# Optimization experiments

Hardware: AMD Instinct MI355X
Metric: run time of the kernel (lower is better)

## Reference

```python
import jax, jax.numpy as jnp
import numpy as np

N, E, B = 150000, 600000, 1024
F_IN, F_HID = 78, 312          # 78 * 2**output_dim_power_0(=2)
OUT_DIM = 128
L, VOCAB, EMB = 1000, 26, 128  # num_features_xt+1 = 26 embedding rows
NF, KS = 8, 8                  # 2**n_filters_power, 2**kernel_size_power
CONV_FLAT = NF * (EMB - KS + 1)  # 8*121 = 968
K_HOPS = 2
SLOPE = 0.01                   # torch leaky_relu default

def _lin(k, i, o):
    s = 1.0 / np.sqrt(i)
    kw, kb = jax.random.split(k)
    return (jax.random.uniform(kw, (i, o), jnp.float32, -s, s),
            jax.random.uniform(kb, (o,), jnp.float32, -s, s))

def setup_inputs() -> dict:
    key = jax.random.key(0)
    ks = jax.random.split(key, 12)
    x = jax.random.normal(ks[0], (N, F_IN), jnp.float32)
    edge_index = jax.random.randint(ks[1], (2, E), 0, N)
    batch = (jnp.arange(N) * B) // N            # sorted graph ids, all B graphs nonempty
    target = jax.random.randint(ks[2], (B, L), 0, VOCAB)
    sgc_w, sgc_b = _lin(ks[3], F_IN, F_HID)
    fcg1_w, fcg1_b = _lin(ks[4], F_HID, OUT_DIM)
    emb_table = jax.random.normal(ks[5], (VOCAB, EMB), jnp.float32)
    sc = 1.0 / np.sqrt(L * KS)
    conv_w = jax.random.uniform(ks[6], (NF, L, KS), jnp.float32, -sc, sc)  # OIW
    conv_b = jax.random.uniform(ks[7], (NF,), jnp.float32, -sc, sc)
    fcxt_w, fcxt_b = _lin(ks[8], CONV_FLAT, OUT_DIM)
    fc1_w, fc1_b = _lin(ks[9], 2 * OUT_DIM, 1024)
    fc2_w, fc2_b = _lin(ks[10], 1024, 512)
    out_w, out_b = _lin(ks[11], 512, 1)
    return dict(x=x, sgc_w=sgc_w, sgc_b=sgc_b, fcg1_w=fcg1_w, fcg1_b=fcg1_b,
                emb_table=emb_table, conv_w=conv_w, conv_b=conv_b,
                fcxt_w=fcxt_w, fcxt_b=fcxt_b, fc1_w=fc1_w, fc1_b=fc1_b,
                fc2_w=fc2_w, fc2_b=fc2_b, out_w=out_w, out_b=out_b,
                edge_index=edge_index, batch=batch, target=target)

def reference(x, sgc_w, sgc_b, fcg1_w, fcg1_b, emb_table, conv_w, conv_b,
              fcxt_w, fcxt_b, fc1_w, fc1_b, fc2_w, fc2_b, out_w, out_b,
              edge_index, batch, target):
    # --- SGConv: K-hop symmetric-normalized propagation with self-loops, then linear ---
    loop = jnp.arange(N)
    src = jnp.concatenate([edge_index[0], loop])
    dst = jnp.concatenate([edge_index[1], loop])
    deg = jax.ops.segment_sum(jnp.ones_like(src, jnp.float32), dst, num_segments=N)
    dinv = jnp.where(deg > 0, jax.lax.rsqrt(deg), 0.0)
    norm = (dinv[src] * dinv[dst])[:, None]
    h = x
    for _ in range(K_HOPS):
        h = jax.ops.segment_sum(h[src] * norm, dst, num_segments=N)  # [N, F]
    h = jax.nn.leaky_relu(h @ sgc_w + sgc_b, SLOPE)                  # [N, 312]
    # --- global max pool per graph + fc_g1 ---
    g = jax.ops.segment_max(h, batch, num_segments=B)                # [B, 312]
    g = jax.nn.leaky_relu(g @ fcg1_w + fcg1_b, SLOPE)                # [B, 128]
    # --- protein branch: embed -> Conv1d(in=1000) over embed axis -> flatten -> fc ---
    emb = emb_table[target]                                          # [B, 1000, 128]
    conv = jax.lax.conv_general_dilated(emb, conv_w, (1,), 'VALID',
                                        dimension_numbers=('NCW', 'OIW', 'NCW'))
    conv = conv + conv_b[None, :, None]                              # [B, 8, 121]
    xt = conv.reshape(B, CONV_FLAT) @ fcxt_w + fcxt_b                # [B, 128]
    # --- head ---
    xc = jnp.concatenate([g, xt], axis=1)                            # [B, 256]
    xc = jax.nn.relu(xc @ fc1_w + fc1_b)
    xc = jax.nn.relu(xc @ fc2_w + fc2_b)
    return xc @ out_w + out_b                                        # [B, 1]
```

## Files before the change

### kernel.cpp

```cpp
#include <hip/hip_runtime.h>

#define N_NODES 150000
#define N_EDGES 600000
#define BATCH   1024
#define F_IN    78
#define F_HID   312
#define OUT_DIMW 128
#define SEQ_L   1000
#define VOCAB   26
#define EMB     128
#define NF      8
#define KS      8
#define CONV_WO 121
#define CONV_FLAT 968
#define SK      208
#define SLOPE   0.01f
#define KEY_NEGMAX ((int)0x80800000)
#define SCAN_NBLK ((N_NODES + 255) / 256)

#define KPU  96
#define NT   20
#define BSW_HALF (3 * NT * 64 * 8)
#define M_PAD 150016

typedef __attribute__((ext_vector_type(8))) short bf8;
typedef __attribute__((ext_vector_type(4))) float f4;

__device__ __forceinline__ short f2bf(float f) {
  unsigned u = __float_as_uint(f);
  return (short)((u + 0x7fffu + ((u >> 16) & 1u)) >> 16);
}
__device__ __forceinline__ float bf2f(short h) {
  return __uint_as_float(((unsigned)(unsigned short)h) << 16);
}
__device__ __forceinline__ unsigned packsplit(float v) {
  short h = f2bf(v);
  short l = f2bf(v - bf2f(h));
  return ((unsigned)(unsigned short)h << 16) | (unsigned)(unsigned short)l;
}

__device__ __forceinline__ int fkey(float v) {
  int i = __float_as_int(v);
  return i >= 0 ? i : (i ^ 0x7fffffff);
}
__device__ __forceinline__ float fdec(int k) {
  return __int_as_float(k >= 0 ? k : (k ^ 0x7fffffff));
}

__global__ void k_zero_i(int* __restrict__ p, int n) {
  int i = blockIdx.x * blockDim.x + threadIdx.x;
  if (i < n) p[i] = 0;
}

__global__ void k_deg(const int* __restrict__ dst, int* __restrict__ deg) {
  int e = blockIdx.x * blockDim.x + threadIdx.x;
  if (e < N_EDGES) atomicAdd(&deg[dst[e]], 1);
}

__global__ void k_dinv(const int* __restrict__ deg, float* __restrict__ dinv) {
  int i = blockIdx.x * blockDim.x + threadIdx.x;
  if (i < N_NODES) dinv[i] = rsqrtf((float)(deg[i] + 1));
}

__global__ __launch_bounds__(256) void k_scan1(const int* __restrict__ deg, int* __restrict__ rowptr,
                                               int* __restrict__ bsum) {
  __shared__ int s[256];
  int tid = threadIdx.x;
  int i = blockIdx.x * 256 + tid;
  int v = (i < N_NODES) ? deg[i] : 0;
  s[tid] = v;
  __syncthreads();
  int x = v;
  for (int o = 1; o < 256; o <<= 1) {
    int t = (tid >= o) ? s[tid - o] : 0;
    __syncthreads();
    x += t; s[tid] = x;
    __syncthreads();
  }
  if (i < N_NODES) rowptr[i] = x - v;
  if (tid == 255) bsum[blockIdx.x] = x;
}

__global__ __launch_bounds__(1024) void k_scan2(int* __restrict__ bsum) {
  __shared__ int s[1024];
  int tid = threadIdx.x;
  int v = (tid < SCAN_NBLK) ? bsum[tid] : 0;
  s[tid] = v;
  __syncthreads();
  int x = v;
  for (int o = 1; o < 1024; o <<= 1) {
    int t = (tid >= o) ? s[tid - o] : 0;
    __syncthreads();
    x += t; s[tid] = x;
    __syncthreads();
  }
  if (tid < SCAN_NBLK) bsum[tid] = x - v;
}

__global__ __launch_bounds__(256) void k_scan3(int* __restrict__ rowptr, const int* __restrict__ bsum,
                                               int* __restrict__ cnt) {
  int i = blockIdx.x * 256 + threadIdx.x;
  if (i < N_NODES) { rowptr[i] += bsum[blockIdx.x]; cnt[i] = 0; }
  if (i == 0) rowptr[N_NODES] = N_EDGES;
}

__global__ void k_fillcsr(const int* __restrict__ src, const int* __restrict__ dst,
                          const int* __restrict__ rowptr, int* __restrict__ cnt,
                          int* __restrict__ csr) {
  int e = blockIdx.x * blockDim.x + threadIdx.x;
  if (e < N_EDGES) {
    int d = dst[e];
    int pos = rowptr[d] + atomicAdd(&cnt[d], 1);
    csr[pos] = src[e];
  }
}

template<int HOP1>
__global__ __launch_bounds__(256) void k_pull(const int* __restrict__ rowptr,
                        const int* __restrict__ csr, const float* __restrict__ dinv,
                        const float* __restrict__ p, void* __restrict__ outv) {
  int dv = (int)((blockIdx.x * 256 + threadIdx.x) >> 6);
  if (dv >= N_NODES) return;
  int d = __builtin_amdgcn_readfirstlane(dv);
  int lane = threadIdx.x & 63;
  int j0 = rowptr[d], j1 = rowptr[d + 1];
  bool act = lane < 39;
  float dd = dinv[d];
  float2 aA = make_float2(0.f, 0.f), aB = aA, aC = aA, aD = aA;
  if (act) {
    float2 v = ((const float2*)(p + (size_t)d * F_IN))[lane];
    float c0 = HOP1 ? dd : 1.f;
    aA.x = c0 * v.x; aA.y = c0 * v.y;
  }
  int j = j0;
  for (; j + 3 < j1; j += 4) {
    int s0 = csr[j], s1 = csr[j + 1], s2 = csr[j + 2], s3 = csr[j + 3];
    float c0 = HOP1 ? dinv[s0] : 1.f, c1 = HOP1 ? dinv[s1] : 1.f;
    float c2 = HOP1 ? dinv[s2] : 1.f, c3 = HOP1 ? dinv[s3] : 1.f;
    if (act) {
      float2 u0 = ((const float2*)(p + (size_t)s0 * F_IN))[lane];
      float2 u1 = ((const float2*)(p + (size_t)s1 * F_IN))[lane];
      float2 u2 = ((const float2*)(p + (size_t)s2 * F_IN))[lane];
      float2 u3 = ((const float2*)(p + (size_t)s3 * F_IN))[lane];
      aA.x += c0 * u0.x; aA.y += c0 * u0.y;
      aB.x += c1 * u1.x; aB.y += c1 * u1.y;
      aC.x += c2 * u2.x; aC.y += c2 * u2.y;
      aD.x += c3 * u3.x; aD.y += c3 * u3.y;
    }
  }
  if (j + 1 < j1) {
    int s0 = csr[j], s1 = csr[j + 1];
    float c0 = HOP1 ? dinv[s0] : 1.f, c1 = HOP1 ? dinv[s1] : 1.f;
    if (act) {
      float2 u0 = ((const float2*)(p + (size_t)s0 * F_IN))[lane];
      float2 u1 = ((const float2*)(p + (size_t)s1 * F_IN))[lane];
      aA.x += c0 * u0.x; aA.y += c0 * u0.y;
      aB.x += c1 * u1.x; aB.y += c1 * u1.y;
    }
    j += 2;
  }
  if (j < j1) {
    int s0 = csr[j];
    float c0 = HOP1 ? dinv[s0] : 1.f;
    if (act) {
      float2 u0 = ((const float2*)(p + (size_t)s0 * F_IN))[lane];
      aC.x += c0 * u0.x; aC.y += c0 * u0.y;
    }
  }
  if (HOP1) {
    if (act) {
      float cs = dd * dd;
      ((float2*)((float*)outv + (size_t)d * F_IN))[lane] =
          make_float2(cs * (aA.x + aB.x + aC.x + aD.x), cs * (aA.y + aB.y + aC.y + aD.y));
    }
  } else {
    if (lane < 48) {
      float vx = dd * (aA.x + aB.x + aC.x + aD.x);
      float vy = dd * (aA.y + aB.y + aC.y + aD.y);
      uint2 pk = make_uint2(packsplit(vx), packsplit(vy));
      ((uint2*)((unsigned*)outv + (size_t)d * KPU))[lane] = pk;
    }
  }
}

__global__ __launch_bounds__(256) void k_gemm_sk(const float* __restrict__ A, const float* __restrict__ B,
                        float* __restrict__ Cp, int M, int N, int K, int kc) {
  __shared__ float As[16][33];
  __shared__ float Bs[16][68];
  int bm = blockIdx.x * 32, bn = blockIdx.y * 64;
  int k0s = blockIdx.z * kc;
  int k1s = min(K, k0s + kc);
  int tid = threadIdx.x;
  int tx = tid & 15, ty = tid >> 4;
  float acc[2][4] = {};
  for (int k0 = k0s; k0 < k1s; k0 += 16) {
    {
      int i2 = tid * 2;
      int m = i2 >> 4, k = i2 & 15;
      float2 av = make_float2(0.f, 0.f);
      const float* Ap = A + (size_t)(bm + m) * K + k0 + k;
      if (k0 + k + 1 < k1s)      av = *(const float2*)Ap;
      else if (k0 + k < k1s)     av.x = Ap[0];
      As[k][m] = av.x; As[k + 1][m] = av.y;
    }
    {
      int i4 = tid * 4;
      int kr = i4 >> 6, n = i4 & 63;
      float4 bv = make_float4(0.f, 0.f, 0.f, 0.f);
      if (k0 + kr < k1s) bv = *(const float4*)(B + (size_t)(k0 + kr) * N + bn + n);
      *(float4*)&Bs[kr][n] = bv;
    }
    __syncthreads();
#pragma unroll
    for (int kk = 0; kk < 16; kk++) {
      float a0 = As[kk][ty * 2], a1 = As[kk][ty * 2 + 1];
      float4 b = *(const float4*)&Bs[kk][tx * 4];
      acc[0][0] += a0 * b.x; acc[0][1] += a0 * b.y; acc[0][2] += a0 * b.z; acc[0][3] += a0 * b.w;
      acc[1][0] += a1 * b.x; acc[1][1] += a1 * b.y; acc[1][2] += a1 * b.z; acc[1][3] += a1 * b.w;
    }
    __syncthreads();
  }
#pragma unroll
  for (int im = 0; im < 2; im++) {
    int m = bm + ty * 2 + im;
    float4 v = make_float4(acc[im][0], acc[im][1], acc[im][2], acc[im][3]);
    *(float4*)(Cp + ((size_t)blockIdx.z * M + m) * N + bn + tx * 4) = v;
  }
}

template<int ACT>
__global__ void k_sumact(const float* __restrict__ Cp, int S, const float* __restrict__ bias,
                         float* __restrict__ C, int nshift, int ldc, int coff) {
  int i = blockIdx.x * 256 + threadIdx.x;
  int MN = gridDim.x * 256;
  int m = i >> nshift, n = i & ((1 << nshift) - 1);
  float s = 0.f;
  for (int t = 0; t < S; t++) s += Cp[(size_t)t * MN + i];
  s += bias[n];
  if (ACT == 1) s = fmaxf(s, 0.f);
  if (ACT == 2) s = s > 0.f ? s : SLOPE * s;
  C[(size_t)m * ldc + coff + n] = s;
}

__global__ void k_bprep(const float* __restrict__ B, short* __restrict__ Bsw,
                        int* __restrict__ gkeys) {
  int i = blockIdx.x * 256 + threadIdx.x;
  if (i < BATCH * F_HID) gkeys[i] = KEY_NEGMAX;
  if (i >= BSW_HALF) return;
  int j = i & 7;
  int lane = (i >> 3) & 63;
  int rest = i >> 9;
  int nt = rest % NT, ksi = rest / NT;
  int n = nt * 16 + (lane & 15);
  int k = ksi * 32 + (lane >> 4) * 8 + j;
  float v = (k < F_IN && n < F_HID) ? B[k * F_HID + n] : 0.f;
  short h = f2bf(v);
  Bsw[i] = h;
  Bsw[BSW_HALF + i] = f2bf(v - bf2f(h));
}

__global__ __launch_bounds__(512) void k_gemm_max(const unsigned* __restrict__ hAp,
                           const short* __restrict__ Bsw,
                           const float* __restrict__ bias, int* __restrict__ gkeys) {
  __shared__ uint4 Bs4[1280];
  __shared__ int red[2 * F_HID];
  int tid = threadIdx.x;
  int m0 = blockIdx.x * 64;

  for (int i = tid; i < 2 * F_HID; i += 512) red[i] = KEY_NEGMAX;

  int w = tid >> 6, lane = tid & 63;
  int stripe = w >> 1, nh = w & 1;
  int mrow = lane & 15, quad = lane >> 4;
  const short* Bss = (const short*)Bs4;
  const uint4* Bq = (const uint4*)Bsw;

  f4 acc[10];
#pragma unroll
  for (int j = 0; j < 10; j++) acc[j] = (f4)0.f;

  for (int ksi = 0; ksi < 3; ksi++) {
    __syncthreads();
    for (int i = tid; i < 1280; i += 512) Bs4[i] = Bq[ksi * 1280 + i];
    __syncthreads();

    const unsigned* ap = hAp + (size_t)(m0 + stripe * 16 + mrow) * KPU + ksi * 32 + quad * 8;
    uint4 u0 = *(const uint4*)ap;
    uint4 u1 = *(const uint4*)(ap + 4);
    unsigned uu[8] = {u0.x, u0.y, u0.z, u0.w, u1.x, u1.y, u1.z, u1.w};
    bf8 ah, al;
#pragma unroll
    for (int j = 0; j < 8; j++) {
      ah[j] = (short)(uu[j] >> 16);
      al[j] = (short)(uu[j] & 0xffffu);
    }
    const short* bb  = Bss + ((size_t)(nh * 10) * 64 + lane) * 8;
    const short* bbg = Bsw + BSW_HALF + ((size_t)(ksi * NT + nh * 10) * 64 + lane) * 8;
#pragma unroll
    for (int j = 0; j < 10; j++) {
      bf8 bl = *(const bf8*)(bbg + j * 512);
      bf8 bh = *(const bf8*)(bb + j * 512);
      acc[j] = __builtin_amdgcn_mfma_f32_16x16x32_bf16(ah, bh, acc[j], 0, 0, 0);
      acc[j] = __builtin_amdgcn_mfma_f32_16x16x32_bf16(al, bh, acc[j], 0, 0, 0);
      acc[j] = __builtin_amdgcn_mfma_f32_16x16x32_bf16(ah, bl, acc[j], 0, 0, 0);
    }
  }

  int g0 = (int)(((long long)m0 * BATCH) / N_NODES);
  int bnd = (int)((((long long)(g0 + 1)) * N_NODES + BATCH - 1) / BATCH);
  int mb = m0 + stripe * 16 + quad * 4;
#pragma unroll
  for (int j = 0; j < 10; j++) {
    int n = (nh * 10 + j) * 16 + mrow;
    bool nok = n < F_HID;
    float bn = nok ? bias[n] : 0.f;
    float mx0 = -3.4e38f, mx1 = -3.4e38f;
#pragma unroll
    for (int r = 0; r < 4; r++) {
      int m = mb + r;
      if (m >= N_NODES) continue;
      float v = acc[j][r] + bn;
      v = v > 0.f ? v : SLOPE * v;
      if (m >= bnd) mx1 = fmaxf(mx1, v); else mx0 = fmaxf(mx0, v);
    }
    mx0 = fmaxf(mx0, __shfl_xor(mx0, 16, 64));
    mx0 = fmaxf(mx0, __shfl_xor(mx0, 32, 64));
    mx1 = fmaxf(mx1, __shfl_xor(mx1, 16, 64));
    mx1 = fmaxf(mx1, __shfl_xor(mx1, 32, 64));
    if (quad == 0 && nok) {
      if (mx0 > -3.3e38f) atomicMax(&red[n], fkey(mx0));
      if (mx1 > -3.3e38f) atomicMax(&red[F_HID + n], fkey(mx1));
    }
  }
  __syncthreads();
  for (int i = tid; i < 2 * F_HID; i += 512) {
    int flag = i / F_HID, n = i - flag * F_HID;
    int g = g0 + flag;
    int key = red[i];
    if (g < BATCH && key != KEY_NEGMAX)
      atomicMax(&gkeys[g * F_HID + n], key);
  }
}

__global__ void k_decode(const int* __restrict__ gkeys, float* __restrict__ g, int n) {
  int i = blockIdx.x * blockDim.x + threadIdx.x;
  if (i < n) g[i] = fdec(gkeys[i]);
}

__global__ __launch_bounds__(256) void k_sbuild(const int* __restrict__ target, const float* __restrict__ conv_w,
                         float* __restrict__ Sg) {
  __shared__ int tl[SEQ_L];
  __shared__ unsigned short order[SEQ_L];
  __shared__ int cnt[VOCAB];
  __shared__ int off[VOCAB + 1];
  __shared__ float Sl[VOCAB * 64];
  int b = blockIdx.x, tid = threadIdx.x;
  for (int l = tid; l < SEQ_L; l += 256) tl[l] = target[b * SEQ_L + l];
  if (tid < VOCAB) cnt[tid] = 0;
  __syncthreads();
  for (int l = tid; l < SEQ_L; l += 256) atomicAdd(&cnt[tl[l]], 1);
  __syncthreads();
  if (tid == 0) { off[0] = 0; for (int v = 0; v < VOCAB; v++) off[v + 1] = off[v] + cnt[v]; }
  __syncthreads();
  if (tid < VOCAB) cnt[tid] = 0;
  __syncthreads();
  for (int l = tid; l < SEQ_L; l += 256) {
    int v = tl[l];
    int p = atomicAdd(&cnt[v], 1);
    order[off[v] + p] = (unsigned short)l;
  }
  for (int i = tid; i < VOCAB * 64; i += 256) Sl[i] = 0.f;
  __syncthreads();
  int fk = tid & 63, q = tid >> 6;
  int f = fk >> 3, k = fk & 7;
  const float* wp = conv_w + f * (SEQ_L * KS) + k;
  for (int v = 0; v < VOCAB; v++) {
    float acc = 0.f;
    for (int j = off[v] + q; j < off[v + 1]; j += 4) {
      int l = order[j];
      acc += wp[l * KS];
    }
    atomicAdd(&Sl[v * 64 + fk], acc);
  }
  __syncthreads();
  for (int i = tid; i < VOCAB * 64; i += 256) {
    int v = i >> 6, fk2 = i & 63;
    int ff = fk2 >> 3, kk = fk2 & 7;
    Sg[((size_t)b * NF + ff) * SK + v * KS + kk] = Sl[i];
  }
}

__global__ __launch_bounds__(256) void k_conv(const float* __restrict__ Sg, const float* __restrict__ emb,
                       const float* __restrict__ conv_b, float* __restrict__ convo) {
  __shared__ float Asub[32][SK];
  __shared__ float Etab[VOCAB * EMB];
  int r0 = blockIdx.x * 32;
  int tid = threadIdx.x;
  float* Af = &Asub[0][0];
  for (int i = tid; i < VOCAB * EMB; i += 256) Etab[i] = emb[i];
  for (int i = tid; i < 32 * SK; i += 256) Af[i] = Sg[(size_t)r0 * SK + i];
  __syncthreads();
  int w = tid & 127;
  int rg = tid >> 7;
  if (w < CONV_WO) {
    float acc[16] = {};
    for (int vk4 = 0; vk4 < SK; vk4 += 4) {
      int v0 = vk4 >> 3, k0 = vk4 & 7;
      float e0 = Etab[v0 * EMB + w + k0];
      float e1 = Etab[v0 * EMB + w + k0 + 1];
      float e2 = Etab[v0 * EMB + w + k0 + 2];
      float e3 = Etab[v0 * EMB + w + k0 + 3];
#pragma unroll
      for (int r = 0; r < 16; r++) {
        float4 a4 = *(const float4*)&Asub[rg * 16 + r][vk4];
        acc[r] += a4.x * e0 + a4.y * e1 + a4.z * e2 + a4.w * e3;
      }
    }
#pragma unroll
    for (int r = 0; r < 16; r++) {
      int row = r0 + rg * 16 + r;
      convo[(size_t)row * CONV_WO + w] = acc[r] + conv_b[row & 7];
    }
  }
}

__global__ void k_out(const float* __restrict__ a2, const float* __restrict__ w,
                      const float* __restrict__ b, float* __restrict__ out) {
  int row = (blockIdx.x * blockDim.x + threadIdx.x) >> 6;
  int lane = threadIdx.x & 63;
  if (row >= BATCH) return;
  const float* ar = a2 + (size_t)row * 512;
  float s = 0.f;
  for (int j = lane; j < 512; j += 64) s += ar[j] * w[j];
  for (int o = 32; o > 0; o >>= 1) s += __shfl_down(s, o, 64);
  if (lane == 0) out[row] = s + b[0];
}

extern "C" void kernel_launch(void* const* d_in, const int* in_sizes, int n_in,
                              void* d_out, int out_size, void* d_ws, size_t ws_size,
                              hipStream_t stream) {
  const float* x      = (const float*)d_in[0];
  const float* sgc_w  = (const float*)d_in[1];
  const float* sgc_b  = (const float*)d_in[2];
  const float* fcg1_w = (const float*)d_in[3];
  const float* fcg1_b = (const float*)d_in[4];
  const float* emb    = (const float*)d_in[5];
  const float* conv_w = (const float*)d_in[6];
  const float* conv_b = (const float*)d_in[7];
  const float* fcxt_w = (const float*)d_in[8];
  const float* fcxt_b = (const float*)d_in[9];
  const float* fc1_w  = (const float*)d_in[10];
  const float* fc1_b  = (const float*)d_in[11];
  const float* fc2_w  = (const float*)d_in[12];
  const float* fc2_b  = (const float*)d_in[13];
  const float* out_w  = (const float*)d_in[14];
  const float* out_b  = (const float*)d_in[15];
  const int* edge     = (const int*)d_in[16];
  const int* target   = (const int*)d_in[18];
  float* out = (float*)d_out;

  char* ws = (char*)d_ws;
  size_t off = 0;
  auto take = [&](size_t bytes) {
    void* p = ws + off;
    off += (bytes + 255) & ~(size_t)255;
    return p;
  };
  int*      deg    = (int*)     take((size_t)N_NODES * 4);
  float*    dinv   = (float*)   take((size_t)N_NODES * 4);
  int*      rowptr = (int*)     take((size_t)(N_NODES + 1) * 4);
  int*      bsum   = (int*)     take((size_t)SCAN_NBLK * 4);
  int*      cnt    = (int*)     take((size_t)N_NODES * 4);
  int*      csr    = (int*)     take((size_t)N_EDGES * 4);
  unsigned* hAp    = (unsigned*)take((size_t)M_PAD * KPU * 4);
  float*    hB     = (float*)   take((size_t)N_NODES * F_IN * 4);
  short*    Bsw    = (short*)   take((size_t)2 * BSW_HALF * 2);
  int*      gkeys  = (int*)     take((size_t)BATCH * F_HID * 4);
  float*    gbuf   = (float*)   take((size_t)BATCH * F_HID * 4);
  float*    Sg     = (float*)   take((size_t)BATCH * NF * SK * 4);
  float*    convo  = (float*)   take((size_t)BATCH * NF * CONV_WO * 4);
  float*    xc     = (float*)   take((size_t)BATCH * 256 * 4);
  float*    a1     = (float*)   take((size_t)BATCH * 1024 * 4);
  float*    a2     = (float*)   take((size_t)BATCH * 512 * 4);
  float*    psum   = hB;

  const int* esrc = edge;
  const int* edst = edge + N_EDGES;

  k_zero_i<<<(N_NODES + 255) / 256, 256, 0, stream>>>(deg, N_NODES);
  k_deg<<<(N_EDGES + 255) / 256, 256, 0, stream>>>(edst, deg);
  k_dinv<<<(N_NODES + 255) / 256, 256, 0, stream>>>(deg, dinv);
  k_scan1<<<SCAN_NBLK, 256, 0, stream>>>(deg, rowptr, bsum);
  k_scan2<<<1, 1024, 0, stream>>>(bsum);
  k_scan3<<<SCAN_NBLK, 256, 0, stream>>>(rowptr, bsum, cnt);
  k_fillcsr<<<(N_EDGES + 255) / 256, 256, 0, stream>>>(esrc, edst, rowptr, cnt, csr);

  k_pull<1><<<(N_NODES * 64 + 255) / 256, 256, 0, stream>>>(rowptr, csr, dinv, x, hB);
  k_pull<0><<<(N_NODES * 64 + 255) / 256, 256, 0, stream>>>(rowptr, csr, dinv, hB, hAp);

  k_bprep<<<(BATCH * F_HID + 255) / 256, 256, 0, stream>>>(sgc_w, Bsw, gkeys);
  k_gemm_max<<<M_PAD / 64, 512, 0, stream>>>(hAp, Bsw, sgc_b, gkeys);
  k_decode<<<(BATCH * F_HID + 255) / 256, 256, 0, stream>>>(gkeys, gbuf, BATCH * F_HID);

  {
    dim3 g(BATCH / 32, OUT_DIMW / 64, 4);
    k_gemm_sk<<<g, 256, 0, stream>>>(gbuf, fcg1_w, psum, BATCH, OUT_DIMW, F_HID, 80);
    k_sumact<2><<<(BATCH * OUT_DIMW) / 256, 256, 0, stream>>>(psum, 4, fcg1_b, xc, 7, 256, 0);
  }

  k_sbuild<<<BATCH, 256, 0, stream>>>(target, conv_w, Sg);
  k_conv<<<(BATCH * NF) / 32, 256, 0, stream>>>(Sg, emb, conv_b, convo);
  {
    dim3 g(BATCH / 32, OUT_DIMW / 64, 8);
    k_gemm_sk<<<g, 256, 0, stream>>>(convo, fcxt_w, psum, BATCH, OUT_DIMW, CONV_FLAT, 128);
    k_sumact<0><<<(BATCH * OUT_DIMW) / 256, 256, 0, stream>>>(psum, 8, fcxt_b, xc, 7, 256, OUT_DIMW);
  }

  {
    dim3 g(BATCH / 32, 1024 / 64, 2);
    k_gemm_sk<<<g, 256, 0, stream>>>(xc, fc1_w, psum, BATCH, 1024, 256, 128);
    k_sumact<1><<<(BATCH * 1024) / 256, 256, 0, stream>>>(psum, 2, fc1_b, a1, 10, 1024, 0);
  }
  {
    dim3 g(BATCH / 32, 512 / 64, 4);
    k_gemm_sk<<<g, 256, 0, stream>>>(a1, fc2_w, psum, BATCH, 512, 1024, 256);
    k_sumact<1><<<(BATCH * 512) / 256, 256, 0, stream>>>(psum, 4, fc2_b, a2, 9, 512, 0);
  }
  k_out<<<(BATCH * 64) / 256, 256, 0, stream>>>(a2, out_w, out_b, out);
}
```

Before: 531.8 us.

## Split hA into hi/lo bf16 planes and retile GEMM-max for B reuse

The pull kernel now writes the bf16 high and low parts of the propagated features into two separate planes instead of interleaved 32-bit pairs. The GEMM-max kernel can then load A fragments directly as bf8 vectors without unpacking. The GEMM-max kernel also drops its LDS staging of B and runs 256 threads, where each wave covers all 4 M-stripes and 5 N-tiles, so every B fragment read from global/L2 is reused across four MFMAs. This removes the block-level syncs and the unpack work, at the cost of more accumulator registers (20 f4) and more B traffic from global memory.

New measurement: 542.6 us. 1.02x slower.

```diff
diff --git a/kernel.cpp b/kernel.cpp
--- a/kernel.cpp
+++ b/kernel.cpp
@@ -22,6 +22,7 @@
 #define NT   20
 #define BSW_HALF (3 * NT * 64 * 8)
 #define M_PAD 150016
+#define HA_PLANE ((size_t)M_PAD * KPU)
 
 typedef __attribute__((ext_vector_type(8))) short bf8;
 typedef __attribute__((ext_vector_type(4))) float f4;
@@ -32,11 +33,6 @@
 }
 __device__ __forceinline__ float bf2f(short h) {
   return __uint_as_float(((unsigned)(unsigned short)h) << 16);
-}
-__device__ __forceinline__ unsigned packsplit(float v) {
-  short h = f2bf(v);
-  short l = f2bf(v - bf2f(h));
-  return ((unsigned)(unsigned short)h << 16) | (unsigned)(unsigned short)l;
 }
 
 __device__ __forceinline__ int fkey(float v) {
@@ -177,8 +173,11 @@
     if (lane < 48) {
       float vx = dd * (aA.x + aB.x + aC.x + aD.x);
       float vy = dd * (aA.y + aB.y + aC.y + aD.y);
-      uint2 pk = make_uint2(packsplit(vx), packsplit(vy));
-      ((uint2*)((unsigned*)outv + (size_t)d * KPU))[lane] = pk;
+      short hx = f2bf(vx); short lx = f2bf(vx - bf2f(hx));
+      short hy = f2bf(vy); short ly = f2bf(vy - bf2f(hy));
+      short* hp = (short*)outv + (size_t)d * KPU;
+      ((short2*)hp)[lane] = make_short2(hx, hy);
+      ((short2*)(hp + HA_PLANE))[lane] = make_short2(lx, ly);
     }
   }
 }
@@ -259,81 +258,80 @@
   Bsw[BSW_HALF + i] = f2bf(v - bf2f(h));
 }
 
-__global__ __launch_bounds__(512) void k_gemm_max(const unsigned* __restrict__ hAp,
+__global__ __launch_bounds__(256) void k_gemm_max(const short* __restrict__ hA,
                            const short* __restrict__ Bsw,
                            const float* __restrict__ bias, int* __restrict__ gkeys) {
-  __shared__ uint4 Bs4[1280];
   __shared__ int red[2 * F_HID];
   int tid = threadIdx.x;
   int m0 = blockIdx.x * 64;
 
-  for (int i = tid; i < 2 * F_HID; i += 512) red[i] = KEY_NEGMAX;
+  for (int i = tid; i < 2 * F_HID; i += 256) red[i] = KEY_NEGMAX;
+  __syncthreads();
 
   int w = tid >> 6, lane = tid & 63;
-  int stripe = w >> 1, nh = w & 1;
   int mrow = lane & 15, quad = lane >> 4;
-  const short* Bss = (const short*)Bs4;
-  const uint4* Bq = (const uint4*)Bsw;
-
-  f4 acc[10];
-#pragma unroll
-  for (int j = 0; j < 10; j++) acc[j] = (f4)0.f;
-
+
+  f4 acc[4][5];
+#pragma unroll
+  for (int mi = 0; mi < 4; mi++)
+#pragma unroll
+    for (int j = 0; j < 5; j++) acc[mi][j] = (f4)0.f;
+
+#pragma unroll
   for (int ksi = 0; ksi < 3; ksi++) {
-    __syncthreads();
-    for (int i = tid; i < 1280; i += 512) Bs4[i] = Bq[ksi * 1280 + i];
-    __syncthreads();
-
-    const unsigned* ap = hAp + (size_t)(m0 + stripe * 16 + mrow) * KPU + ksi * 32 + quad * 8;
-    uint4 u0 = *(const uint4*)ap;
-    uint4 u1 = *(const uint4*)(ap + 4);
-    unsigned uu[8] = {u0.x, u0.y, u0.z, u0.w, u1.x, u1.y, u1.z, u1.w};
-    bf8 ah, al;
-#pragma unroll
-    for (int j = 0; j < 8; j++) {
-      ah[j] = (short)(uu[j] >> 16);
-      al[j] = (short)(uu[j] & 0xffffu);
-    }
-    const short* bb  = Bss + ((size_t)(nh * 10) * 64 + lane) * 8;
-    const short* bbg = Bsw + BSW_HALF + ((size_t)(ksi * NT + nh * 10) * 64 + lane) * 8;
-#pragma unroll
-    for (int j = 0; j < 10; j++) {
-      bf8 bl = *(const bf8*)(bbg + j * 512);
-      bf8 bh = *(const bf8*)(bb + j * 512);
-      acc[j] = __builtin_amdgcn_mfma_f32_16x16x32_bf16(ah, bh, acc[j], 0, 0, 0);
-      acc[j] = __builtin_amdgcn_mfma_f32_16x16x32_bf16(al, bh, acc[j], 0, 0, 0);
-      acc[j] = __builtin_amdgcn_mfma_f32_16x16x32_bf16(ah, bl, acc[j], 0, 0, 0);
+    bf8 ah[4], al[4];
+#pragma unroll
+    for (int mi = 0; mi < 4; mi++) {
+      const short* ap = hA + (size_t)(m0 + mi * 16 + mrow) * KPU + ksi * 32 + quad * 8;
+      ah[mi] = *(const bf8*)ap;
+      al[mi] = *(const bf8*)(ap + HA_PLANE);
+    }
+    const short* bh = Bsw + ((size_t)(ksi * NT + w * 5) * 64 + lane) * 8;
+    const short* bl = bh + BSW_HALF;
+#pragma unroll
+    for (int j = 0; j < 5; j++) {
+      bf8 bhv = *(const bf8*)(bh + j * 512);
+      bf8 blv = *(const bf8*)(bl + j * 512);
+#pragma unroll
+      for (int mi = 0; mi < 4; mi++) {
+        acc[mi][j] = __builtin_amdgcn_mfma_f32_16x16x32_bf16(ah[mi], bhv, acc[mi][j], 0, 0, 0);
+        acc[mi][j] = __builtin_amdgcn_mfma_f32_16x16x32_bf16(al[mi], bhv, acc[mi][j], 0, 0, 0);
+        acc[mi][j] = __builtin_amdgcn_mfma_f32_16x16x32_bf16(ah[mi], blv, acc[mi][j], 0, 0, 0);
+      }
     }
   }
 
   int g0 = (int)(((long long)m0 * BATCH) / N_NODES);
   int bnd = (int)((((long long)(g0 + 1)) * N_NODES + BATCH - 1) / BATCH);
-  int mb = m0 + stripe * 16 + quad * 4;
-#pragma unroll
-  for (int j = 0; j < 10; j++) {
-    int n = (nh * 10 + j) * 16 + mrow;
+#pragma unroll
+  for (int j = 0; j < 5; j++) {
+    int n = (w * 5 + j) * 16 + mrow;
     bool nok = n < F_HID;
     float bn = nok ? bias[n] : 0.f;
-    float mx0 = -3.4e38f, mx1 = -3.4e38f;
-#pragma unroll
-    for (int r = 0; r < 4; r++) {
-      int m = mb + r;
-      if (m >= N_NODES) continue;
-      float v = acc[j][r] + bn;
-      v = v > 0.f ? v : SLOPE * v;
-      if (m >= bnd) mx1 = fmaxf(mx1, v); else mx0 = fmaxf(mx0, v);
-    }
-    mx0 = fmaxf(mx0, __shfl_xor(mx0, 16, 64));
-    mx0 = fmaxf(mx0, __shfl_xor(mx0, 32, 64));
-    mx1 = fmaxf(mx1, __shfl_xor(mx1, 16, 64));
-    mx1 = fmaxf(mx1, __shfl_xor(mx1, 32, 64));
-    if (quad == 0 && nok) {
-      if (mx0 > -3.3e38f) atomicMax(&red[n], fkey(mx0));
-      if (mx1 > -3.3e38f) atomicMax(&red[F_HID + n], fkey(mx1));
-    }
-  }
-  __syncthreads();
-  for (int i = tid; i < 2 * F_HID; i += 512) {
+#pragma unroll
+    for (int mi = 0; mi < 4; mi++) {
+      int mb = m0 + mi * 16 + quad * 4;
+      float mx0 = -3.4e38f, mx1 = -3.4e38f;
+#pragma unroll
+      for (int r = 0; r < 4; r++) {
+        int m = mb + r;
+        if (m >= N_NODES) continue;
+        float v = acc[mi][j][r] + bn;
+        v = v > 0.f ? v : SLOPE * v;
+        if (m >= bnd) mx1 = fmaxf(mx1, v); else mx0 = fmaxf(mx0, v);
+      }
+      mx0 = fmaxf(mx0, __shfl_xor(mx0, 16, 64));
+      mx0 = fmaxf(mx0, __shfl_xor(mx0, 32, 64));
+      mx1 = fmaxf(mx1, __shfl_xor(mx1, 16, 64));
+      mx1 = fmaxf(mx1, __shfl_xor(mx1, 32, 64));
+      if (quad == 0 && nok) {
+        if (mx0 > -3.3e38f) atomicMax(&red[n], fkey(mx0));
+        if (mx1 > -3.3e38f) atomicMax(&red[F_HID + n], fkey(mx1));
+      }
+    }
+  }
+  __syncthreads();
+  for (int i = tid; i < 2 * F_HID; i += 256) {
     int flag = i / F_HID, n = i - flag * F_HID;
     int g = g0 + flag;
     int key = red[i];
@@ -472,7 +470,7 @@
   int*      bsum   = (int*)     take((size_t)SCAN_NBLK * 4);
   int*      cnt    = (int*)     take((size_t)N_NODES * 4);
   int*      csr    = (int*)     take((size_t)N_EDGES * 4);
-  unsigned* hAp    = (unsigned*)take((size_t)M_PAD * KPU * 4);
+  short*    hA     = (short*)   take((size_t)M_PAD * KPU * 4);
   float*    hB     = (float*)   take((size_t)N_NODES * F_IN * 4);
   short*    Bsw    = (short*)   take((size_t)2 * BSW_HALF * 2);
   int*      gkeys  = (int*)     take((size_t)BATCH * F_HID * 4);
@@ -496,10 +494,10 @@
   k_fillcsr<<<(N_EDGES + 255) / 256, 256, 0, stream>>>(esrc, edst, rowptr, cnt, csr);
 
   k_pull<1><<<(N_NODES * 64 + 255) / 256, 256, 0, stream>>>(rowptr, csr, dinv, x, hB);
-  k_pull<0><<<(N_NODES * 64 + 255) / 256, 256, 0, stream>>>(rowptr, csr, dinv, hB, hAp);
+  k_pull<0><<<(N_NODES * 64 + 255) / 256, 256, 0, stream>>>(rowptr, csr, dinv, hB, hA);
 
   k_bprep<<<(BATCH * F_HID + 255) / 256, 256, 0, stream>>>(sgc_w, Bsw, gkeys);
-  k_gemm_max<<<M_PAD / 64, 512, 0, stream>>>(hAp, Bsw, sgc_b, gkeys);
+  k_gemm_max<<<M_PAD / 64, 256, 0, stream>>>(hA, Bsw, sgc_b, gkeys);
   k_decode<<<(BATCH * F_HID + 255) / 256, 256, 0, stream>>>(gkeys, gbuf, BATCH * F_HID);
 
   {
```
